# Performance work log

Measured on AMD Instinct MI355X. Metric: run time of the kernel, lower is better.

## Reference

```python
import jax, jax.numpy as jnp
import numpy as np

D = 1024
H = 16
DH = D // H


def setup_inputs() -> dict:
    key = jax.random.key(0)
    ks = jax.random.split(key, 9)
    s = 1.0 / np.sqrt(D)
    return {
        "x": jax.random.normal(ks[0], (4, 2048, D), dtype=jnp.float32),
        "wq": jax.random.uniform(ks[1], (D, D), jnp.float32, -s, s),
        "bq": jax.random.uniform(ks[2], (D,), jnp.float32, -s, s),
        "wk": jax.random.uniform(ks[3], (D, D), jnp.float32, -s, s),
        "bk": jax.random.uniform(ks[4], (D,), jnp.float32, -s, s),
        "wv": jax.random.uniform(ks[5], (D, D), jnp.float32, -s, s),
        "bv": jax.random.uniform(ks[6], (D,), jnp.float32, -s, s),
        "wo": jax.random.uniform(ks[7], (D, D), jnp.float32, -s, s),
        "bo": jax.random.uniform(ks[8], (D,), jnp.float32, -s, s),
    }


def reference(x, wq, bq, wk, bk, wv, bv, wo, bo):
    B, S, _ = x.shape
    # projections + split heads: [B, S, D] -> [B, H, S, Dh]
    def split(t):
        return t.reshape(B, S, H, DH).transpose(0, 2, 1, 3)
    q = split(x @ wq + bq)
    k = split(x @ wk + bk)
    v = split(x @ wv + bv)
    scale = 1.0 / jnp.sqrt(jnp.float32(DH))
    scores = jnp.einsum("bhqd,bhkd->bhqk", q, k) * scale  # [B,H,S,S]
    att = jax.nn.softmax(scores, axis=-1)
    out = jnp.einsum("bhqk,bhkd->bhqd", att, v)  # [B,H,S,Dh]
    out = out.transpose(0, 2, 1, 3).reshape(B, S, D)
    return out @ wo + bo
```

## Files before the change

### kernel.cpp

```cpp
#include <hip/hip_runtime.h>
#include <stdint.h>

typedef float f32x4 __attribute__((ext_vector_type(4)));
typedef __bf16 bf16x8 __attribute__((ext_vector_type(8)));
typedef unsigned short ushort_t;
typedef ushort_t ushortx8 __attribute__((ext_vector_type(8)));

#define DEV static __device__ __forceinline__

DEV ushort_t f2bf(float f) {
  union { float f; uint32_t u; } v; v.f = f;
  uint32_t u = v.u;
  return (ushort_t)((u + 0x7FFFu + ((u >> 16) & 1u)) >> 16);
}

DEV uint32_t pkbf(float a, float b) {
  __bf16 x = (__bf16)a, y = (__bf16)b;
  return (uint32_t)__builtin_bit_cast(unsigned short, x) |
         ((uint32_t)__builtin_bit_cast(unsigned short, y) << 16);
}

DEV void cp16(const void* g, void* l) {
  __builtin_amdgcn_global_load_lds((const __attribute__((address_space(1))) unsigned int*)g,
                                   (__attribute__((address_space(3))) unsigned int*)l,
                                   16, 0, 0);
}

DEV f32x4 mfma16(bf16x8 a, bf16x8 b, f32x4 c) {
  return __builtin_amdgcn_mfma_f32_16x16x32_bf16(a, b, c, 0, 0, 0);
}

__global__ __launch_bounds__(256) void k_cvt_x(const float* __restrict__ x,
                                               ushort_t* __restrict__ xb) {
  size_t idx = ((size_t)blockIdx.x * 256 + threadIdx.x) * 8;
  const float4* src = (const float4*)(x + idx);
  float4 a = src[0], b = src[1];
  ushortx8 o;
  o[0] = f2bf(a.x); o[1] = f2bf(a.y); o[2] = f2bf(a.z); o[3] = f2bf(a.w);
  o[4] = f2bf(b.x); o[5] = f2bf(b.y); o[6] = f2bf(b.z); o[7] = f2bf(b.w);
  *(ushortx8*)(xb + idx) = o;
}

__global__ __launch_bounds__(256) void k_transpose_w(const float* __restrict__ src,
                                                     ushort_t* __restrict__ dst) {
  __shared__ float tile[32][33];
  int tx = threadIdx.x & 31, ty = threadIdx.x >> 5;
  int c0 = blockIdx.x * 32, r0 = blockIdx.y * 32;
#pragma unroll
  for (int i = ty; i < 32; i += 8)
    tile[i][tx] = src[(size_t)(r0 + i) * 1024 + c0 + tx];
  __syncthreads();
#pragma unroll
  for (int i = ty; i < 32; i += 8)
    dst[(size_t)(c0 + i) * 1024 + r0 + tx] = f2bf(tile[tx][i]);
}

template <int MODE>
__global__ __launch_bounds__(256, 2) void k_gemm(
    const ushort_t* __restrict__ A, const ushort_t* __restrict__ Bt,
    const float* __restrict__ b0, const float* __restrict__ b1,
    const float* __restrict__ b2, ushort_t* __restrict__ qw,
    ushort_t* __restrict__ kw, ushort_t* __restrict__ vtw,
    float* __restrict__ outf) {
  const int K = 1024;
  __shared__ ushort_t As[128 * 32];
  __shared__ ushort_t Bs[128 * 32];
  int tid = threadIdx.x;
  int w = tid >> 6, lane = tid & 63, l16 = lane & 15, lg = lane >> 4;
  int m0 = blockIdx.x * 128, n0 = blockIdx.y * 128;
  int wm = (w >> 1) * 64, wn = (w & 1) * 64;
  f32x4 acc[4][4] = {};

  const ushort_t* Ag = A + (size_t)(m0 + (tid >> 2)) * K + (tid & 3) * 8;
  const ushort_t* Bg = Bt + (size_t)(n0 + (tid >> 2)) * K + (tid & 3) * 8;

  for (int k0 = 0; k0 < K; k0 += 32) {
    cp16(Ag + k0, As + w * 512);
    cp16(Ag + k0 + 64 * K, As + 2048 + w * 512);
    cp16(Bg + k0, Bs + w * 512);
    cp16(Bg + k0 + 64 * K, Bs + 2048 + w * 512);
    __syncthreads();
    bf16x8 af[4], bfr[4];
#pragma unroll
    for (int i = 0; i < 4; ++i)
      af[i] = *(const bf16x8*)&As[(wm + i * 16 + l16) * 32 + lg * 8];
#pragma unroll
    for (int j = 0; j < 4; ++j)
      bfr[j] = *(const bf16x8*)&Bs[(wn + j * 16 + l16) * 32 + lg * 8];
#pragma unroll
    for (int i = 0; i < 4; ++i)
#pragma unroll
      for (int j = 0; j < 4; ++j)
        acc[i][j] = mfma16(af[i], bfr[j], acc[i][j]);
    __syncthreads();
  }

  if (MODE == 0) {
    const float QSCALE = 0.18033688011112042f;
    int p = n0 >> 10;
    const float* bias = (p == 0) ? b0 : (p == 1) ? b1 : b2;
    int c0 = n0 & 1023;
#pragma unroll
    for (int j = 0; j < 4; ++j) {
      int col = c0 + wn + j * 16 + l16;
      float bb = bias[col];
      int h = col >> 6, dh = col & 63;
#pragma unroll
      for (int i = 0; i < 4; ++i) {
#pragma unroll
        for (int r = 0; r < 4; ++r) {
          int row = m0 + wm + i * 16 + lg * 4 + r;
          int bi = row >> 11, s = row & 2047;
          float val = acc[i][j][r] + bb;
          if (p == 0)
            qw[((size_t)(bi * 16 + h) * 2048 + s) * 64 + dh] = f2bf(val * QSCALE);
          else if (p == 1)
            kw[((size_t)(bi * 16 + h) * 2048 + s) * 64 + dh] = f2bf(val);
          else
            vtw[((size_t)(bi * 16 + h) * 64 + dh) * 2048 + s] = f2bf(val);
        }
      }
    }
  } else {
#pragma unroll
    for (int j = 0; j < 4; ++j) {
      int col = n0 + wn + j * 16 + l16;
      float bb = b0[col];
#pragma unroll
      for (int i = 0; i < 4; ++i) {
#pragma unroll
        for (int r = 0; r < 4; ++r) {
          int row = m0 + wm + i * 16 + lg * 4 + r;
          outf[(size_t)row * 1024 + col] = acc[i][j][r] + bb;
        }
      }
    }
  }
}

__global__ __launch_bounds__(256, 3) void k_attn(
    const ushort_t* __restrict__ qg, const ushort_t* __restrict__ kg,
    const ushort_t* __restrict__ vtg, ushort_t* __restrict__ att) {
  __shared__ ushort_t Ks[128 * 64];
  __shared__ ushort_t Vs[64 * 128];
  __shared__ ushort_t Ps[4][16 * 136];
  int tid = threadIdx.x;
  int w = tid >> 6, lane = tid & 63, l16 = lane & 15, lg = lane >> 4;
  int i = blockIdx.x;
  int bh = (i & 7) * 8 + ((i >> 3) & 7);
  int q0 = (i >> 6) * 128;
  const ushort_t* qh = qg + (size_t)bh * 2048 * 64;

  int rK = w * 8 + (lane >> 3);
  int cK = (lane & 7) ^ (rK & 7);
  const ushort_t* kstage = kg + (size_t)bh * 2048 * 64 + (size_t)rK * 64 + cK * 8;
  int rV = w * 4 + (lane >> 4);
  int cV = (lane & 15) ^ (rV & 15);
  const ushort_t* vstage = vtg + (size_t)bh * 64 * 2048 + (size_t)rV * 2048 + cV * 8;

  bf16x8 qf[2][2];
#pragma unroll
  for (int st = 0; st < 2; ++st)
#pragma unroll
    for (int ks = 0; ks < 2; ++ks)
      qf[st][ks] = *(const bf16x8*)(qh + (size_t)(q0 + w * 32 + st * 16 + l16) * 64 +
                                    ks * 32 + lg * 8);

  bf16x8 vone;
#pragma unroll
  for (int t = 0; t < 8; ++t) vone[t] = (__bf16)1.0f;

  f32x4 o[2][5] = {};

  for (int kb = 0; kb < 2048; kb += 128) {
    __syncthreads();
#pragma unroll
    for (int j = 0; j < 4; ++j) {
      cp16(kstage + (size_t)(kb + j * 32) * 64, Ks + (j * 256 + w * 64) * 8);
      cp16(vstage + kb + (size_t)j * 16 * 2048, Vs + (j * 256 + w * 64) * 8);
    }
    __syncthreads();

    f32x4 sc[2][8] = {};
#pragma unroll
    for (int jt = 0; jt < 8; ++jt) {
      int row = jt * 16 + l16;
      bf16x8 kf0 = *(const bf16x8*)&Ks[row * 64 + ((lg) ^ (l16 & 7)) * 8];
      bf16x8 kf1 = *(const bf16x8*)&Ks[row * 64 + ((lg + 4) ^ (l16 & 7)) * 8];
      sc[0][jt] = mfma16(kf0, qf[0][0], sc[0][jt]);
      sc[0][jt] = mfma16(kf1, qf[0][1], sc[0][jt]);
      sc[1][jt] = mfma16(kf0, qf[1][0], sc[1][jt]);
      sc[1][jt] = mfma16(kf1, qf[1][1], sc[1][jt]);
    }

#pragma unroll
    for (int st = 0; st < 2; ++st) {
#pragma unroll
      for (int jt = 0; jt < 8; ++jt) {
        float e0 = __builtin_amdgcn_exp2f(sc[st][jt][0]);
        float e1 = __builtin_amdgcn_exp2f(sc[st][jt][1]);
        float e2 = __builtin_amdgcn_exp2f(sc[st][jt][2]);
        float e3 = __builtin_amdgcn_exp2f(sc[st][jt][3]);
        uint32_t* dst = (uint32_t*)&Ps[w][l16 * 136 + jt * 16 + lg * 4];
        dst[0] = pkbf(e0, e1);
        dst[1] = pkbf(e2, e3);
      }
#pragma unroll
      for (int ks = 0; ks < 4; ++ks) {
        bf16x8 pf = *(const bf16x8*)&Ps[w][l16 * 136 + ks * 32 + lg * 8];
#pragma unroll
        for (int dt = 0; dt < 4; ++dt) {
          int vrow = dt * 16 + l16;
          bf16x8 vf =
              *(const bf16x8*)&Vs[vrow * 128 + ((ks * 4 + lg) ^ (l16 & 15)) * 8];
          o[st][dt] = mfma16(pf, vf, o[st][dt]);
        }
        o[st][4] = mfma16(pf, vone, o[st][4]);
      }
    }
  }

  int bi = bh >> 4, h = bh & 15;
#pragma unroll
  for (int st = 0; st < 2; ++st) {
    f32x4 inv;
#pragma unroll
    for (int r = 0; r < 4; ++r) inv[r] = __builtin_amdgcn_rcpf(o[st][4][r]);
#pragma unroll
    for (int dt = 0; dt < 4; ++dt)
#pragma unroll
      for (int r = 0; r < 4; ++r) {
        int srow = q0 + w * 32 + st * 16 + lg * 4 + r;
        int col = h * 64 + dt * 16 + l16;
        att[(size_t)(bi * 2048 + srow) * 1024 + col] = f2bf(o[st][dt][r] * inv[r]);
      }
  }
}

extern "C" void kernel_launch(void* const* d_in, const int* in_sizes, int n_in,
                              void* d_out, int out_size, void* d_ws, size_t ws_size,
                              hipStream_t stream) {
  const float* x = (const float*)d_in[0];
  const float* wq = (const float*)d_in[1];
  const float* bq = (const float*)d_in[2];
  const float* wk = (const float*)d_in[3];
  const float* bk = (const float*)d_in[4];
  const float* wv = (const float*)d_in[5];
  const float* bv = (const float*)d_in[6];
  const float* wo = (const float*)d_in[7];
  const float* bo = (const float*)d_in[8];
  float* out = (float*)d_out;

  char* ws = (char*)d_ws;
  ushort_t* xb = (ushort_t*)(ws);
  ushort_t* wqkvT = (ushort_t*)(ws + 16777216);
  ushort_t* woT = (ushort_t*)(ws + 23068672);
  ushort_t* qw = (ushort_t*)(ws + 25165824);
  ushort_t* kw = (ushort_t*)(ws + 41943040);
  ushort_t* vtw = (ushort_t*)(ws + 58720256);
  ushort_t* att = (ushort_t*)(ws + 75497472);

  k_cvt_x<<<dim3(4096), dim3(256), 0, stream>>>(x, xb);
  k_transpose_w<<<dim3(32, 32), dim3(256), 0, stream>>>(wq, wqkvT);
  k_transpose_w<<<dim3(32, 32), dim3(256), 0, stream>>>(wk, wqkvT + 1024 * 1024);
  k_transpose_w<<<dim3(32, 32), dim3(256), 0, stream>>>(wv, wqkvT + 2 * 1024 * 1024);
  k_transpose_w<<<dim3(32, 32), dim3(256), 0, stream>>>(wo, woT);

  k_gemm<0><<<dim3(64, 24), dim3(256), 0, stream>>>(
      xb, wqkvT, bq, bk, bv, qw, kw, vtw, nullptr);

  k_attn<<<dim3(1024), dim3(256), 0, stream>>>(qw, kw, vtw, att);

  k_gemm<1><<<dim3(64, 8), dim3(256), 0, stream>>>(
      att, woT, bo, nullptr, nullptr, nullptr, nullptr, nullptr, out);
}
```

Baseline: 319.4 us.

## Swap QKV GEMM operands for vectorized stores, add V transpose, widen attention blocks

The QKV projection now computes the transposed product, so each lane holds 4 consecutive head-dim values and writes them as one 8-byte packed store instead of scattered 2-byte stores. The V output is written in row layout to scratch and then transposed by a new LDS-tiled kernel, replacing the strided transposed write. The attention kernel moves to 512 threads covering 256 queries per block, computes scores per subtile to lower register pressure, and uses an XOR-swizzled P buffer in place of a padded one. The cost is an extra kernel launch and an extra round trip of V through memory.

```diff
diff --git a/kernel.cpp b/kernel.cpp
--- a/kernel.cpp
+++ b/kernel.cpp
@@ -5,6 +5,7 @@
 typedef __bf16 bf16x8 __attribute__((ext_vector_type(8)));
 typedef unsigned short ushort_t;
 typedef ushort_t ushortx8 __attribute__((ext_vector_type(8)));
+typedef ushort_t ushortx4 __attribute__((ext_vector_type(4)));
 
 #define DEV static __device__ __forceinline__
 
@@ -55,12 +56,34 @@
     dst[(size_t)(c0 + i) * 1024 + r0 + tx] = f2bf(tile[tx][i]);
 }
 
+__global__ __launch_bounds__(256) void k_transpose_v(const ushort_t* __restrict__ vw,
+                                                     ushort_t* __restrict__ vtw) {
+  __shared__ ushort_t t[64][72];
+  int tid = threadIdx.x;
+  int bh = blockIdx.y, s0 = blockIdx.x * 64;
+#pragma unroll
+  for (int n = 0; n < 2; ++n) {
+    int row = (tid >> 3) + n * 32, ch = (tid & 7) * 8;
+    *(ushortx8*)&t[row][ch] =
+        *(const ushortx8*)&vw[((size_t)bh * 2048 + s0 + row) * 64 + ch];
+  }
+  __syncthreads();
+#pragma unroll
+  for (int n = 0; n < 2; ++n) {
+    int dh = (tid >> 3) + n * 32, sc = (tid & 7) * 8;
+    ushortx8 o;
+#pragma unroll
+    for (int k = 0; k < 8; ++k) o[k] = t[sc + k][dh];
+    *(ushortx8*)&vtw[((size_t)bh * 64 + dh) * 2048 + s0 + sc] = o;
+  }
+}
+
 template <int MODE>
 __global__ __launch_bounds__(256, 2) void k_gemm(
     const ushort_t* __restrict__ A, const ushort_t* __restrict__ Bt,
     const float* __restrict__ b0, const float* __restrict__ b1,
     const float* __restrict__ b2, ushort_t* __restrict__ qw,
-    ushort_t* __restrict__ kw, ushort_t* __restrict__ vtw,
+    ushort_t* __restrict__ kw, ushort_t* __restrict__ vw,
     float* __restrict__ outf) {
   const int K = 1024;
   __shared__ ushort_t As[128 * 32];
@@ -97,28 +120,27 @@
 
   if (MODE == 0) {
     const float QSCALE = 0.18033688011112042f;
-    int p = n0 >> 10;
+    int p = m0 >> 10;
     const float* bias = (p == 0) ? b0 : (p == 1) ? b1 : b2;
-    int c0 = n0 & 1023;
-#pragma unroll
-    for (int j = 0; j < 4; ++j) {
-      int col = c0 + wn + j * 16 + l16;
-      float bb = bias[col];
-      int h = col >> 6, dh = col & 63;
-#pragma unroll
-      for (int i = 0; i < 4; ++i) {
-#pragma unroll
-        for (int r = 0; r < 4; ++r) {
-          int row = m0 + wm + i * 16 + lg * 4 + r;
-          int bi = row >> 11, s = row & 2047;
-          float val = acc[i][j][r] + bb;
-          if (p == 0)
-            qw[((size_t)(bi * 16 + h) * 2048 + s) * 64 + dh] = f2bf(val * QSCALE);
-          else if (p == 1)
-            kw[((size_t)(bi * 16 + h) * 2048 + s) * 64 + dh] = f2bf(val);
-          else
-            vtw[((size_t)(bi * 16 + h) * 64 + dh) * 2048 + s] = f2bf(val);
-        }
+    ushort_t* dst = (p == 0) ? qw : (p == 1) ? kw : vw;
+    float qs = (p == 0) ? QSCALE : 1.0f;
+    int cbase = m0 & 1023;
+#pragma unroll
+    for (int i = 0; i < 4; ++i) {
+      int oc = cbase + wm + i * 16 + lg * 4;
+      int h = oc >> 6, dh0 = oc & 63;
+      float4 bb = *(const float4*)&bias[oc];
+#pragma unroll
+      for (int j = 0; j < 4; ++j) {
+        int tok = n0 + wn + j * 16 + l16;
+        size_t base =
+            ((size_t)((tok >> 11) * 16 + h) * 2048 + (tok & 2047)) * 64 + dh0;
+        ushortx4 pk;
+        pk[0] = f2bf((acc[i][j][0] + bb.x) * qs);
+        pk[1] = f2bf((acc[i][j][1] + bb.y) * qs);
+        pk[2] = f2bf((acc[i][j][2] + bb.z) * qs);
+        pk[3] = f2bf((acc[i][j][3] + bb.w) * qs);
+        *(ushortx4*)&dst[base] = pk;
       }
     }
   } else {
@@ -138,25 +160,23 @@
   }
 }
 
-__global__ __launch_bounds__(256, 3) void k_attn(
+__global__ __launch_bounds__(512, 4) void k_attn(
     const ushort_t* __restrict__ qg, const ushort_t* __restrict__ kg,
     const ushort_t* __restrict__ vtg, ushort_t* __restrict__ att) {
   __shared__ ushort_t Ks[128 * 64];
   __shared__ ushort_t Vs[64 * 128];
-  __shared__ ushort_t Ps[4][16 * 136];
+  __shared__ ushort_t Ps[8][16 * 128];
   int tid = threadIdx.x;
   int w = tid >> 6, lane = tid & 63, l16 = lane & 15, lg = lane >> 4;
   int i = blockIdx.x;
   int bh = (i & 7) * 8 + ((i >> 3) & 7);
-  int q0 = (i >> 6) * 128;
+  int q0 = (i >> 6) * 256;
   const ushort_t* qh = qg + (size_t)bh * 2048 * 64;
 
-  int rK = w * 8 + (lane >> 3);
-  int cK = (lane & 7) ^ (rK & 7);
-  const ushort_t* kstage = kg + (size_t)bh * 2048 * 64 + (size_t)rK * 64 + cK * 8;
-  int rV = w * 4 + (lane >> 4);
-  int cV = (lane & 15) ^ (rV & 15);
-  const ushort_t* vstage = vtg + (size_t)bh * 64 * 2048 + (size_t)rV * 2048 + cV * 8;
+  const ushort_t* kstage = kg + (size_t)bh * 2048 * 64 + (size_t)(tid >> 3) * 64 +
+                           (size_t)(((tid & 7) ^ ((tid >> 3) & 7)) * 8);
+  const ushort_t* vstage = vtg + (size_t)bh * 64 * 2048 + (size_t)(tid >> 4) * 2048 +
+                           (size_t)(((tid & 15) ^ ((tid >> 4) & 15)) * 8);
 
   bf16x8 qf[2][2];
 #pragma unroll
@@ -174,45 +194,44 @@
 
   for (int kb = 0; kb < 2048; kb += 128) {
     __syncthreads();
-#pragma unroll
-    for (int j = 0; j < 4; ++j) {
-      cp16(kstage + (size_t)(kb + j * 32) * 64, Ks + (j * 256 + w * 64) * 8);
-      cp16(vstage + kb + (size_t)j * 16 * 2048, Vs + (j * 256 + w * 64) * 8);
-    }
-    __syncthreads();
-
-    f32x4 sc[2][8] = {};
-#pragma unroll
-    for (int jt = 0; jt < 8; ++jt) {
-      int row = jt * 16 + l16;
-      bf16x8 kf0 = *(const bf16x8*)&Ks[row * 64 + ((lg) ^ (l16 & 7)) * 8];
-      bf16x8 kf1 = *(const bf16x8*)&Ks[row * 64 + ((lg + 4) ^ (l16 & 7)) * 8];
-      sc[0][jt] = mfma16(kf0, qf[0][0], sc[0][jt]);
-      sc[0][jt] = mfma16(kf1, qf[0][1], sc[0][jt]);
-      sc[1][jt] = mfma16(kf0, qf[1][0], sc[1][jt]);
-      sc[1][jt] = mfma16(kf1, qf[1][1], sc[1][jt]);
-    }
+    cp16(kstage + (size_t)kb * 64, Ks + w * 512);
+    cp16(kstage + (size_t)(kb + 64) * 64, Ks + 4096 + w * 512);
+    cp16(vstage + kb, Vs + w * 512);
+    cp16(vstage + kb + (size_t)32 * 2048, Vs + 4096 + w * 512);
+    __syncthreads();
 
 #pragma unroll
     for (int st = 0; st < 2; ++st) {
+      f32x4 sc[8] = {};
 #pragma unroll
       for (int jt = 0; jt < 8; ++jt) {
-        float e0 = __builtin_amdgcn_exp2f(sc[st][jt][0]);
-        float e1 = __builtin_amdgcn_exp2f(sc[st][jt][1]);
-        float e2 = __builtin_amdgcn_exp2f(sc[st][jt][2]);
-        float e3 = __builtin_amdgcn_exp2f(sc[st][jt][3]);
-        uint32_t* dst = (uint32_t*)&Ps[w][l16 * 136 + jt * 16 + lg * 4];
+        int row = jt * 16 + l16;
+        bf16x8 kf0 = *(const bf16x8*)&Ks[row * 64 + ((lg) ^ (l16 & 7)) * 8];
+        bf16x8 kf1 = *(const bf16x8*)&Ks[row * 64 + ((lg + 4) ^ (l16 & 7)) * 8];
+        sc[jt] = mfma16(kf0, qf[st][0], sc[jt]);
+        sc[jt] = mfma16(kf1, qf[st][1], sc[jt]);
+      }
+#pragma unroll
+      for (int jt = 0; jt < 8; ++jt) {
+        float e0 = __builtin_amdgcn_exp2f(sc[jt][0]);
+        float e1 = __builtin_amdgcn_exp2f(sc[jt][1]);
+        float e2 = __builtin_amdgcn_exp2f(sc[jt][2]);
+        float e3 = __builtin_amdgcn_exp2f(sc[jt][3]);
+        uint32_t* dst = (uint32_t*)&Ps[w][l16 * 128 +
+                                         (((jt * 2 + (lg >> 1)) ^ l16) * 8) +
+                                         (lg & 1) * 4];
         dst[0] = pkbf(e0, e1);
         dst[1] = pkbf(e2, e3);
       }
 #pragma unroll
       for (int ks = 0; ks < 4; ++ks) {
-        bf16x8 pf = *(const bf16x8*)&Ps[w][l16 * 136 + ks * 32 + lg * 8];
+        bf16x8 pf =
+            *(const bf16x8*)&Ps[w][l16 * 128 + (((ks * 4 + lg) ^ l16) * 8)];
 #pragma unroll
         for (int dt = 0; dt < 4; ++dt) {
           int vrow = dt * 16 + l16;
           bf16x8 vf =
-              *(const bf16x8*)&Vs[vrow * 128 + ((ks * 4 + lg) ^ (l16 & 15)) * 8];
+              *(const bf16x8*)&Vs[vrow * 128 + (((ks * 4 + lg) ^ l16) * 8)];
           o[st][dt] = mfma16(pf, vf, o[st][dt]);
         }
         o[st][4] = mfma16(pf, vone, o[st][4]);
@@ -259,6 +278,7 @@
   ushort_t* kw = (ushort_t*)(ws + 41943040);
   ushort_t* vtw = (ushort_t*)(ws + 58720256);
   ushort_t* att = (ushort_t*)(ws + 75497472);
+  ushort_t* vw = att;
 
   k_cvt_x<<<dim3(4096), dim3(256), 0, stream>>>(x, xb);
   k_transpose_w<<<dim3(32, 32), dim3(256), 0, stream>>>(wq, wqkvT);
@@ -266,10 +286,12 @@
   k_transpose_w<<<dim3(32, 32), dim3(256), 0, stream>>>(wv, wqkvT + 2 * 1024 * 1024);
   k_transpose_w<<<dim3(32, 32), dim3(256), 0, stream>>>(wo, woT);
 
-  k_gemm<0><<<dim3(64, 24), dim3(256), 0, stream>>>(
-      xb, wqkvT, bq, bk, bv, qw, kw, vtw, nullptr);
-
-  k_attn<<<dim3(1024), dim3(256), 0, stream>>>(qw, kw, vtw, att);
+  k_gemm<0><<<dim3(24, 64), dim3(256), 0, stream>>>(
+      wqkvT, xb, bq, bk, bv, qw, kw, vw, nullptr);
+
+  k_transpose_v<<<dim3(32, 64), dim3(256), 0, stream>>>(vw, vtw);
+
+  k_attn<<<dim3(512), dim3(512), 0, stream>>>(qw, kw, vtw, att);
 
   k_gemm<1><<<dim3(64, 8), dim3(256), 0, stream>>>(
       att, woT, bo, nullptr, nullptr, nullptr, nullptr, nullptr, out);
```

Result: faster. 296.3 us (-7.2%).
